# Kernel tuning notes

Measured on AMD Instinct MI355X. Metric: run time of the kernel, lower is better.

Reference implementation:

```python
import jax, jax.numpy as jnp
import numpy as np

TARGET_RADIUS = 0.99
EPS = 1e-8


def _effective_W_h(W_h):
    """Spectral-norm constraint: 3 power iterations (no grad through u,v),
    then rescale W_h so its spectral radius is TARGET_RADIUS."""
    dim = W_h.shape[0]
    u = jax.random.normal(jax.random.key(1), (dim,), dtype=W_h.dtype)
    u = u / jnp.linalg.norm(u)
    Ws = jax.lax.stop_gradient(W_h)
    v = None
    for _ in range(3):
        v = Ws.T @ u
        v = v / (jnp.linalg.norm(v) + EPS)
        u = Ws @ v
        u = u / (jnp.linalg.norm(u) + EPS)
    sigma = jnp.abs(u @ W_h @ v)  # grad flows only through W_h here
    return W_h * (TARGET_RADIUS / (sigma + EPS))


def setup_inputs() -> dict:
    key = jax.random.key(0)
    ks = jax.random.split(key, 6)
    T, B, D = 2048, 16, 1024
    xavier = float(np.sqrt(6.0 / (D + D)))
    return {
        "x": jax.random.normal(ks[0], (T, B, D), dtype=jnp.float32),
        "h0": jnp.zeros((B, D), dtype=jnp.float32),
        "W_x": jax.random.uniform(ks[1], (D, D), jnp.float32, -xavier, xavier),
        "W_h": jax.random.uniform(ks[2], (D, D), jnp.float32, -xavier, xavier),
        "W_delta": jax.random.uniform(ks[3], (D, D), jnp.float32, -0.1 * xavier, 0.1 * xavier),
        "b": jnp.zeros((D,), dtype=jnp.float32),
        "b_delta": jnp.full((D,), -2.0, dtype=jnp.float32),
        "b_gate": jnp.zeros((D,), dtype=jnp.float32),
    }


def reference(x, h0, W_x, W_h, W_delta, b, b_delta, b_gate):
    # x: [T, B, D]; h0: [B, D]
    W_h_eff = _effective_W_h(W_h)
    # Batch the input-side GEMMs over all timesteps at once.
    delta_raw = jnp.einsum("tbd,ed->tbe", x, W_delta) + b_delta  # [T,B,D]
    cand_x = jnp.einsum("tbd,ed->tbe", x, W_x) + b               # [T,B,D]

    def step(h_prev, inputs):
        x_t, dr_t, cx_t = inputs
        delta = jax.nn.sigmoid(dr_t)
        candidate = jnp.tanh(cx_t + h_prev @ W_h_eff.T)
        h_new = (1.0 - delta) * h_prev + delta * candidate
        out_t = h_new * jax.nn.silu(h_new + x_t + b_gate)
        return h_new, (out_t, h_new)

    _, (output, hs) = jax.lax.scan(step, h0, (x, delta_raw, cand_x))
    h = jnp.concatenate([h0[None], hs], axis=0)  # [T+1, B, D]
    return output, h
```

## Files before the change

kernel.cpp:

```cpp
#include <hip/hip_runtime.h>
#include <hip/hip_fp16.h>
#include <stdint.h>

#define TT 2048
#define BB 16
#define DD 1024
static const size_t H0OFF = 33554432;

typedef _Float16 f16;
typedef _Float16 f16x2 __attribute__((ext_vector_type(2)));
typedef _Float16 f16x8 __attribute__((ext_vector_type(8)));
typedef float f32x4 __attribute__((ext_vector_type(4)));

__device__ __forceinline__ float erfinv_xla(float x) {
  float w = -log1pf(-x * x);
  float p;
  if (w < 5.0f) {
    w -= 2.5f;
    p = 2.81022636e-08f;
    p = fmaf(p, w, 3.43273939e-07f);
    p = fmaf(p, w, -3.5233877e-06f);
    p = fmaf(p, w, -4.39150654e-06f);
    p = fmaf(p, w, 0.00021858087f);
    p = fmaf(p, w, -0.00125372503f);
    p = fmaf(p, w, -0.00417768164f);
    p = fmaf(p, w, 0.246640727f);
    p = fmaf(p, w, 1.50140941f);
  } else {
    w = sqrtf(w) - 3.0f;
    p = -0.000200214257f;
    p = fmaf(p, w, 0.000100950558f);
    p = fmaf(p, w, 0.00134934322f);
    p = fmaf(p, w, -0.00367342844f);
    p = fmaf(p, w, 0.00573950773f);
    p = fmaf(p, w, -0.0076224613f);
    p = fmaf(p, w, 0.00943887047f);
    p = fmaf(p, w, 1.00167406f);
    p = fmaf(p, w, 2.83297682f);
  }
  return p * x;
}

__device__ __forceinline__ float bits_to_normal(unsigned bits) {
  unsigned fb = (bits >> 9) | 0x3f800000u;
  float f = __uint_as_float(fb) - 1.0f;
  const float lo = -0.99999994f;
  float u = f * 2.0f + lo;
  u = fmaxf(lo, u);
  return __uint_as_float(0x3fb504f3u) * erfinv_xla(u);
}

#define TF_ROUND(r) { x0 += x1; x1 = (x1 << r) | (x1 >> (32 - r)); x1 ^= x0; }

__global__ void k_u0(float* t0, float* u) {
  __shared__ float red[512];
  int i = threadIdx.x;
  unsigned ks0 = 0u, ks1 = 1u, ks2 = 0x1BD11BDAu ^ 0u ^ 1u;
  unsigned x0 = (unsigned)i + ks0;
  unsigned x1 = (unsigned)(i + 512) + ks1;
  TF_ROUND(13) TF_ROUND(15) TF_ROUND(26) TF_ROUND(6)
  x0 += ks1; x1 += ks2 + 1u;
  TF_ROUND(17) TF_ROUND(29) TF_ROUND(16) TF_ROUND(24)
  x0 += ks2; x1 += ks0 + 2u;
  TF_ROUND(13) TF_ROUND(15) TF_ROUND(26) TF_ROUND(6)
  x0 += ks0; x1 += ks1 + 3u;
  TF_ROUND(17) TF_ROUND(29) TF_ROUND(16) TF_ROUND(24)
  x0 += ks1; x1 += ks2 + 4u;
  TF_ROUND(13) TF_ROUND(15) TF_ROUND(26) TF_ROUND(6)
  x0 += ks2; x1 += ks0 + 5u;
  float z0 = bits_to_normal(x0);
  float z1 = bits_to_normal(x1);
  t0[i] = z0; t0[i + 512] = z1;
  red[i] = z0 * z0 + z1 * z1;
  __syncthreads();
  for (int s = 256; s > 0; s >>= 1) { if (i < s) red[i] += red[i + s]; __syncthreads(); }
  float inv = 1.0f / sqrtf(red[0]);
  u[i] = t0[i] * inv; u[i + 512] = t0[i + 512] * inv;
}

__global__ void k_mvT(const float* __restrict__ W, const float* __restrict__ u,
                      float* __restrict__ out) {
  int j = blockIdx.x * 256 + threadIdx.x;
  float acc = 0.f;
  for (int i = 0; i < DD; ++i) acc = fmaf(W[(size_t)i * DD + j], u[i], acc);
  out[j] = acc;
}

__global__ void k_mv(const float* __restrict__ W, const float* __restrict__ v,
                     float* __restrict__ out) {
  int gtid = blockIdx.x * 256 + threadIdx.x;
  int wave = gtid >> 6, lane = threadIdx.x & 63;
  for (int rr = 0; rr < 16; ++rr) {
    int row = wave * 16 + rr;
    float acc = 0.f;
    for (int c = 0; c < 16; ++c) {
      int col = c * 64 + lane;
      acc = fmaf(W[(size_t)row * DD + col], v[col], acc);
    }
    for (int off = 32; off > 0; off >>= 1) acc += __shfl_down(acc, off, 64);
    if (lane == 0) out[row] = acc;
  }
}

__global__ void k_norm(const float* __restrict__ src, float* __restrict__ dst, float eps) {
  __shared__ float red[1024];
  int i = threadIdx.x;
  float xv = src[i];
  red[i] = xv * xv;
  __syncthreads();
  for (int s = 512; s > 0; s >>= 1) { if (i < s) red[i] += red[i + s]; __syncthreads(); }
  float inv = 1.0f / (sqrtf(red[0]) + eps);
  dst[i] = src[i] * inv;
}

__global__ void k_sigma(const float* __restrict__ u, const float* __restrict__ wv,
                        float* __restrict__ scale) {
  __shared__ float red[1024];
  int i = threadIdx.x;
  red[i] = u[i] * wv[i];
  __syncthreads();
  for (int s = 512; s > 0; s >>= 1) { if (i < s) red[i] += red[i + s]; __syncthreads(); }
  if (i == 0) scale[0] = 0.99f / (fabsf(red[0]) + 1e-8f);
}

__global__ void k_castWh(const float* __restrict__ Wh, const float* __restrict__ scale,
                         f16* __restrict__ WhH) {
  int i = blockIdx.x * 256 + threadIdx.x;
  float s = scale[0];
  WhH[i] = (f16)(Wh[i] * s);
}

__global__ __launch_bounds__(256) void k_gemm(const float* __restrict__ X,
                                              const float* __restrict__ Wt,
                                              const float* __restrict__ bias,
                                              float* __restrict__ Cout) {
  __shared__ __align__(16) f16 Ah[128 * 64];
  __shared__ __align__(16) f16 Bh[128 * 64];
  int m0 = blockIdx.x * 128, n0 = blockIdx.y * 128;
  int tid = threadIdx.x, lane = tid & 63, w = tid >> 6;
  int wm = w & 1, wn = w >> 1;
  int srow = tid >> 3, scol = (tid & 7) * 8;
  f32x4 acc[4][4];
#pragma unroll
  for (int i = 0; i < 4; ++i)
#pragma unroll
    for (int j = 0; j < 4; ++j) acc[i][j] = (f32x4){0.f, 0.f, 0.f, 0.f};

  for (int kt = 0; kt < 16; ++kt) {
    int k0 = kt * 64;
#pragma unroll
    for (int c = 0; c < 4; ++c) {
      int row = c * 32 + srow;
      const float4* sa = (const float4*)(X + (size_t)(m0 + row) * DD + k0 + scol);
      float4 a0 = sa[0], a1 = sa[1];
      f16x8 hv;
      hv[0] = (f16)a0.x; hv[1] = (f16)a0.y; hv[2] = (f16)a0.z; hv[3] = (f16)a0.w;
      hv[4] = (f16)a1.x; hv[5] = (f16)a1.y; hv[6] = (f16)a1.z; hv[7] = (f16)a1.w;
      *(f16x8*)&Ah[row * 64 + scol] = hv;
      const float4* sb = (const float4*)(Wt + (size_t)(n0 + row) * DD + k0 + scol);
      float4 b0 = sb[0], b1 = sb[1];
      f16x8 hw;
      hw[0] = (f16)b0.x; hw[1] = (f16)b0.y; hw[2] = (f16)b0.z; hw[3] = (f16)b0.w;
      hw[4] = (f16)b1.x; hw[5] = (f16)b1.y; hw[6] = (f16)b1.z; hw[7] = (f16)b1.w;
      *(f16x8*)&Bh[row * 64 + scol] = hw;
    }
    __syncthreads();
#pragma unroll
    for (int ks = 0; ks < 2; ++ks) {
      f16x8 af[4], bf[4];
#pragma unroll
      for (int i = 0; i < 4; ++i)
        af[i] = *(const f16x8*)&Ah[(wm * 64 + i * 16 + (lane & 15)) * 64 + ks * 32 + (lane >> 4) * 8];
#pragma unroll
      for (int j = 0; j < 4; ++j)
        bf[j] = *(const f16x8*)&Bh[(wn * 64 + j * 16 + (lane & 15)) * 64 + ks * 32 + (lane >> 4) * 8];
#pragma unroll
      for (int i = 0; i < 4; ++i)
#pragma unroll
        for (int j = 0; j < 4; ++j)
          acc[i][j] = __builtin_amdgcn_mfma_f32_16x16x32_f16(af[i], bf[j], acc[i][j], 0, 0, 0);
    }
    __syncthreads();
  }
#pragma unroll
  for (int j = 0; j < 4; ++j) {
    int col = n0 + wn * 64 + j * 16 + (lane & 15);
    float bs = bias[col];
#pragma unroll
    for (int i = 0; i < 4; ++i) {
      int rbase = m0 + wm * 64 + i * 16 + (lane >> 4) * 4;
#pragma unroll
      for (int r = 0; r < 4; ++r)
        Cout[(size_t)(rbase + r) * DD + col] = acc[i][j][r] + bs;
    }
  }
}

__device__ __forceinline__ float fdot2f(f16x2 a, f16x2 b, float c) {
#if __has_builtin(__builtin_amdgcn_fdot2)
  return __builtin_amdgcn_fdot2(a, b, c, false);
#else
  return c + (float)a[0] * (float)b[0] + (float)a[1] * (float)b[1];
#endif
}

__device__ __forceinline__ float sigmoid_fast(float v) {
  return 1.0f / (1.0f + __expf(-v));
}
__device__ __forceinline__ float tanh_fast(float v) {
  float t = __expf(-2.0f * fabsf(v));
  float r = (1.0f - t) / (1.0f + t);
  return copysignf(r, v);
}

__global__ __launch_bounds__(256, 1) void k_rec(const float* __restrict__ x,
                                                const float* __restrict__ h0,
                                                const float* __restrict__ b_gate,
                                                const f16* __restrict__ WhH,
                                                uint32_t* __restrict__ hx,
                                                float* __restrict__ d_out) {
  int bid = blockIdx.x;
  int batch = bid & 15;
  int eslice = bid >> 4;
  int tid = threadIdx.x, lane = tid & 63, wv = tid >> 6;
  int e0 = eslice * 64;
  int e = e0 + lane;

  __shared__ __align__(16) uint32_t hsh[512];
  __shared__ float partial[4][64];

  f16x2 wreg[128];
  const f16* wrow = WhH + (size_t)e * DD + wv * 256;
#pragma unroll
  for (int k = 0; k < 128; ++k) wreg[k] = *(const f16x2*)(wrow + 2 * k);

  {
    const float* hb = h0 + (size_t)batch * DD + 4 * tid;
    float a0 = hb[0], a1 = hb[1], a2 = hb[2], a3 = hb[3];
    f16x2 p0; p0[0] = (f16)a0; p0[1] = (f16)a1;
    f16x2 p1; p1[0] = (f16)a2; p1[1] = (f16)a3;
    hsh[2 * tid]     = __builtin_bit_cast(uint32_t, p0);
    hsh[2 * tid + 1] = __builtin_bit_cast(uint32_t, p1);
  }
  float h_own = 0.f, bgv = 0.f, cx_c = 0.f, dr_c = 0.f, xv_c = 0.f;
  if (wv == 0) {
    h_own = h0[(size_t)batch * DD + e];
    bgv = b_gate[e];
    d_out[H0OFF + (size_t)batch * DD + e] = h_own;
    size_t base0 = (size_t)batch * DD + e;
    cx_c = d_out[base0];
    dr_c = d_out[H0OFF + 16384 + base0];
    xv_c = x[base0];
  }
  __syncthreads();

#pragma unroll 1
  for (int t = 0; t < TT; ++t) {
    float cx_n = 0.f, dr_n = 0.f, xv_n = 0.f;
    if (wv == 0 && t + 1 < TT) {
      size_t basen = (size_t)(t + 1) * 16384 + (size_t)batch * DD + e;
      cx_n = d_out[basen];
      dr_n = d_out[H0OFF + 16384 + basen];
      xv_n = x[basen];
    }
    float acc = 0.f;
#pragma unroll
    for (int k4 = 0; k4 < 32; ++k4) {
      uint4 q = *(((const uint4*)hsh) + wv * 32 + k4);
      acc = fdot2f(wreg[k4 * 4 + 0], __builtin_bit_cast(f16x2, q.x), acc);
      acc = fdot2f(wreg[k4 * 4 + 1], __builtin_bit_cast(f16x2, q.y), acc);
      acc = fdot2f(wreg[k4 * 4 + 2], __builtin_bit_cast(f16x2, q.z), acc);
      acc = fdot2f(wreg[k4 * 4 + 3], __builtin_bit_cast(f16x2, q.w), acc);
    }
    partial[wv][lane] = acc;
    __syncthreads();

    uint32_t want = (uint32_t)(t + 1);
    uint32_t* slot = hx + (size_t)(want & 15u) * (BB * DD) + (size_t)batch * DD;

    if (wv == 0) {
      float hdot = partial[0][lane] + partial[1][lane] + partial[2][lane] + partial[3][lane];
      float dlt = sigmoid_fast(dr_c);
      float cand = tanh_fast(cx_c + hdot);
      float hn = (1.f - dlt) * h_own + dlt * cand;
      uint16_t hb16 = __builtin_bit_cast(uint16_t, (f16)hn);
      __hip_atomic_store(&slot[e], (want << 16) | (uint32_t)hb16,
                         __ATOMIC_RELAXED, __HIP_MEMORY_SCOPE_AGENT);
      size_t base = (size_t)t * 16384 + (size_t)batch * DD + e;
      float z = hn + xv_c + bgv;
      d_out[base] = hn * z * sigmoid_fast(z);
      d_out[H0OFF + 16384 + base] = hn;
      h_own = hn; cx_c = cx_n; dr_c = dr_n; xv_c = xv_n;
    }

    if (t + 1 < TT) {
      uint32_t* wp = slot + 4 * tid;
      uint32_t w0, w1, w2, w3;
      while (true) {
        w0 = __hip_atomic_load(wp + 0, __ATOMIC_RELAXED, __HIP_MEMORY_SCOPE_AGENT);
        w1 = __hip_atomic_load(wp + 1, __ATOMIC_RELAXED, __HIP_MEMORY_SCOPE_AGENT);
        w2 = __hip_atomic_load(wp + 2, __ATOMIC_RELAXED, __HIP_MEMORY_SCOPE_AGENT);
        w3 = __hip_atomic_load(wp + 3, __ATOMIC_RELAXED, __HIP_MEMORY_SCOPE_AGENT);
        if (((w0 >> 16) == want) && ((w1 >> 16) == want) &&
            ((w2 >> 16) == want) && ((w3 >> 16) == want)) break;
      }
      hsh[2 * tid]     = (w0 & 0xffffu) | (w1 << 16);
      hsh[2 * tid + 1] = (w2 & 0xffffu) | (w3 << 16);
      __syncthreads();
    }
  }
}

extern "C" void kernel_launch(void* const* d_in, const int* in_sizes, int n_in,
                              void* d_out_v, int out_size, void* d_ws, size_t ws_size,
                              hipStream_t stream) {
  const float* x  = (const float*)d_in[0];
  const float* h0 = (const float*)d_in[1];
  const float* Wx = (const float*)d_in[2];
  const float* Wh = (const float*)d_in[3];
  const float* Wd = (const float*)d_in[4];
  const float* b  = (const float*)d_in[5];
  const float* bd = (const float*)d_in[6];
  const float* bg = (const float*)d_in[7];
  float* out = (float*)d_out_v;

  char* ws = (char*)d_ws;
  float* u    = (float*)(ws + 0);
  float* v    = (float*)(ws + 4096);
  float* t0   = (float*)(ws + 8192);
  float* sc   = (float*)(ws + 12288);
  uint32_t* hx = (uint32_t*)(ws + 65536);
  f16* WhH  = (f16*)(ws + 2097152);

  hipMemsetAsync(hx, 0, (size_t)16 * BB * DD * 4, stream);

  k_u0<<<1, 512, 0, stream>>>(t0, u);
  for (int it = 0; it < 3; ++it) {
    k_mvT<<<4, 256, 0, stream>>>(Wh, u, t0);
    k_norm<<<1, 1024, 0, stream>>>(t0, v, 1e-8f);
    k_mv<<<16, 256, 0, stream>>>(Wh, v, t0);
    k_norm<<<1, 1024, 0, stream>>>(t0, u, 1e-8f);
  }
  k_sigma<<<1, 1024, 0, stream>>>(u, t0, sc);
  k_castWh<<<4096, 256, 0, stream>>>(Wh, sc, WhH);

  dim3 gg(256, 8, 1);
  k_gemm<<<gg, 256, 0, stream>>>(x, Wx, b, out);
  k_gemm<<<gg, 256, 0, stream>>>(x, Wd, bd, out + H0OFF + 16384);

  k_rec<<<256, 256, 0, stream>>>(x, h0, bg, WhH, hx, out);
}
```

Measured before the change: 4.262 ms.

## Make recurrent h exchange wave-local and spread the step epilogue across all waves

Each wave now polls and loads only the 256-element slice of the new hidden state that its own dot products use, and writes it to its own region of shared memory. This drops the block-wide barrier at the end of every timestep, and the partial-sum buffer is double-buffered so a single barrier per step is enough. The per-element epilogue work is split across 16 lanes of each of the four waves instead of running only in wave 0. The dot product uses four independent accumulators for more instruction-level parallelism. Polling becomes a two-phase wave-uniform check with s_sleep, which may add some wake-up latency on the critical path.

```diff
diff --git a/kernel.cpp b/kernel.cpp
--- a/kernel.cpp
+++ b/kernel.cpp
@@ -196,11 +196,13 @@
   }
 }
 
-__device__ __forceinline__ float fdot2f(f16x2 a, f16x2 b, float c) {
+__device__ __forceinline__ float fdot2u(uint32_t a, uint32_t b, float c) {
 #if __has_builtin(__builtin_amdgcn_fdot2)
-  return __builtin_amdgcn_fdot2(a, b, c, false);
+  return __builtin_amdgcn_fdot2(__builtin_bit_cast(f16x2, a),
+                                __builtin_bit_cast(f16x2, b), c, false);
 #else
-  return c + (float)a[0] * (float)b[0] + (float)a[1] * (float)b[1];
+  f16x2 av = __builtin_bit_cast(f16x2, a), bv = __builtin_bit_cast(f16x2, b);
+  return c + (float)av[0] * (float)bv[0] + (float)av[1] * (float)bv[1];
 #endif
 }
 
@@ -223,70 +225,90 @@
   int batch = bid & 15;
   int eslice = bid >> 4;
   int tid = threadIdx.x, lane = tid & 63, wv = tid >> 6;
-  int e0 = eslice * 64;
-  int e = e0 + lane;
-
-  __shared__ __align__(16) uint32_t hsh[512];
-  __shared__ float partial[4][64];
-
-  f16x2 wreg[128];
-  const f16* wrow = WhH + (size_t)e * DD + wv * 256;
-#pragma unroll
-  for (int k = 0; k < 128; ++k) wreg[k] = *(const f16x2*)(wrow + 2 * k);
-
+
+  __shared__ __align__(16) uint16_t hsh[1024];
+  __shared__ float partial[2][4][64];
+
+  uint4 wq[32];
   {
-    const float* hb = h0 + (size_t)batch * DD + 4 * tid;
-    float a0 = hb[0], a1 = hb[1], a2 = hb[2], a3 = hb[3];
-    f16x2 p0; p0[0] = (f16)a0; p0[1] = (f16)a1;
-    f16x2 p1; p1[0] = (f16)a2; p1[1] = (f16)a3;
-    hsh[2 * tid]     = __builtin_bit_cast(uint32_t, p0);
-    hsh[2 * tid + 1] = __builtin_bit_cast(uint32_t, p1);
-  }
+    const uint4* wp = (const uint4*)(WhH + (size_t)(64 * eslice + lane) * DD + 256 * wv);
+#pragma unroll
+    for (int k = 0; k < 32; ++k) wq[k] = wp[k];
+  }
+
+#pragma unroll
+  for (int k = 0; k < 4; ++k) {
+    int g = 256 * wv + 64 * k + lane;
+    hsh[g] = __builtin_bit_cast(uint16_t, (f16)h0[(size_t)batch * DD + g]);
+  }
+
   float h_own = 0.f, bgv = 0.f, cx_c = 0.f, dr_c = 0.f, xv_c = 0.f;
-  if (wv == 0) {
-    h_own = h0[(size_t)batch * DD + e];
-    bgv = b_gate[e];
-    d_out[H0OFF + (size_t)batch * DD + e] = h_own;
-    size_t base0 = (size_t)batch * DD + e;
-    cx_c = d_out[base0];
-    dr_c = d_out[H0OFF + 16384 + base0];
-    xv_c = x[base0];
-  }
-  __syncthreads();
+  int e_g = 0;
+  if (lane < 16) {
+    int rr = 16 * wv + lane;
+    e_g = 64 * eslice + rr;
+    size_t b0 = (size_t)batch * DD + e_g;
+    h_own = h0[b0];
+    bgv = b_gate[e_g];
+    d_out[H0OFF + b0] = h_own;
+    cx_c = d_out[b0];
+    dr_c = d_out[H0OFF + 16384 + b0];
+    xv_c = x[b0];
+  }
+  asm volatile("s_waitcnt lgkmcnt(0)" ::: "memory");
 
 #pragma unroll 1
   for (int t = 0; t < TT; ++t) {
     float cx_n = 0.f, dr_n = 0.f, xv_n = 0.f;
-    if (wv == 0 && t + 1 < TT) {
-      size_t basen = (size_t)(t + 1) * 16384 + (size_t)batch * DD + e;
-      cx_n = d_out[basen];
-      dr_n = d_out[H0OFF + 16384 + basen];
-      xv_n = x[basen];
-    }
-    float acc = 0.f;
-#pragma unroll
-    for (int k4 = 0; k4 < 32; ++k4) {
-      uint4 q = *(((const uint4*)hsh) + wv * 32 + k4);
-      acc = fdot2f(wreg[k4 * 4 + 0], __builtin_bit_cast(f16x2, q.x), acc);
-      acc = fdot2f(wreg[k4 * 4 + 1], __builtin_bit_cast(f16x2, q.y), acc);
-      acc = fdot2f(wreg[k4 * 4 + 2], __builtin_bit_cast(f16x2, q.z), acc);
-      acc = fdot2f(wreg[k4 * 4 + 3], __builtin_bit_cast(f16x2, q.w), acc);
-    }
-    partial[wv][lane] = acc;
+    if (lane < 16 && t + 1 < TT) {
+      size_t bn = (size_t)(t + 1) * 16384 + (size_t)batch * DD + e_g;
+      cx_n = d_out[bn];
+      dr_n = d_out[H0OFF + 16384 + bn];
+      xv_n = x[bn];
+    }
+
+    const uint4* hq = (const uint4*)hsh;
+    float a0 = 0.f, a1 = 0.f, a2 = 0.f, a3 = 0.f;
+#pragma unroll
+    for (int k = 0; k < 32; k += 4) {
+      {
+        uint4 q = hq[32 * wv + k + 0]; uint4 wqq = wq[k + 0];
+        a0 = fdot2u(wqq.x, q.x, a0); a0 = fdot2u(wqq.y, q.y, a0);
+        a0 = fdot2u(wqq.z, q.z, a0); a0 = fdot2u(wqq.w, q.w, a0);
+      }
+      {
+        uint4 q = hq[32 * wv + k + 1]; uint4 wqq = wq[k + 1];
+        a1 = fdot2u(wqq.x, q.x, a1); a1 = fdot2u(wqq.y, q.y, a1);
+        a1 = fdot2u(wqq.z, q.z, a1); a1 = fdot2u(wqq.w, q.w, a1);
+      }
+      {
+        uint4 q = hq[32 * wv + k + 2]; uint4 wqq = wq[k + 2];
+        a2 = fdot2u(wqq.x, q.x, a2); a2 = fdot2u(wqq.y, q.y, a2);
+        a2 = fdot2u(wqq.z, q.z, a2); a2 = fdot2u(wqq.w, q.w, a2);
+      }
+      {
+        uint4 q = hq[32 * wv + k + 3]; uint4 wqq = wq[k + 3];
+        a3 = fdot2u(wqq.x, q.x, a3); a3 = fdot2u(wqq.y, q.y, a3);
+        a3 = fdot2u(wqq.z, q.z, a3); a3 = fdot2u(wqq.w, q.w, a3);
+      }
+    }
+    partial[t & 1][wv][lane] = (a0 + a1) + (a2 + a3);
     __syncthreads();
 
     uint32_t want = (uint32_t)(t + 1);
-    uint32_t* slot = hx + (size_t)(want & 15u) * (BB * DD) + (size_t)batch * DD;
-
-    if (wv == 0) {
-      float hdot = partial[0][lane] + partial[1][lane] + partial[2][lane] + partial[3][lane];
+    uint32_t* sl = hx + (size_t)(want & 15u) * (BB * DD) + (size_t)batch * DD;
+
+    if (lane < 16) {
+      int rr = 16 * wv + lane;
+      const float* pp = &partial[t & 1][0][rr];
+      float hdot = (pp[0] + pp[64]) + (pp[128] + pp[192]);
       float dlt = sigmoid_fast(dr_c);
       float cand = tanh_fast(cx_c + hdot);
       float hn = (1.f - dlt) * h_own + dlt * cand;
-      uint16_t hb16 = __builtin_bit_cast(uint16_t, (f16)hn);
-      __hip_atomic_store(&slot[e], (want << 16) | (uint32_t)hb16,
+      uint16_t hb = __builtin_bit_cast(uint16_t, (f16)hn);
+      __hip_atomic_store(&sl[e_g], (want << 16) | (uint32_t)hb,
                          __ATOMIC_RELAXED, __HIP_MEMORY_SCOPE_AGENT);
-      size_t base = (size_t)t * 16384 + (size_t)batch * DD + e;
+      size_t base = (size_t)t * 16384 + (size_t)batch * DD + e_g;
       float z = hn + xv_c + bgv;
       d_out[base] = hn * z * sigmoid_fast(z);
       d_out[H0OFF + 16384 + base] = hn;
@@ -294,19 +316,30 @@
     }
 
     if (t + 1 < TT) {
-      uint32_t* wp = slot + 4 * tid;
-      uint32_t w0, w1, w2, w3;
+      int sidx = 256 * wv + 64 * (lane >> 2) + 16 * (lane & 3);
       while (true) {
-        w0 = __hip_atomic_load(wp + 0, __ATOMIC_RELAXED, __HIP_MEMORY_SCOPE_AGENT);
-        w1 = __hip_atomic_load(wp + 1, __ATOMIC_RELAXED, __HIP_MEMORY_SCOPE_AGENT);
-        w2 = __hip_atomic_load(wp + 2, __ATOMIC_RELAXED, __HIP_MEMORY_SCOPE_AGENT);
-        w3 = __hip_atomic_load(wp + 3, __ATOMIC_RELAXED, __HIP_MEMORY_SCOPE_AGENT);
-        if (((w0 >> 16) == want) && ((w1 >> 16) == want) &&
-            ((w2 >> 16) == want) && ((w3 >> 16) == want)) break;
-      }
-      hsh[2 * tid]     = (w0 & 0xffffu) | (w1 << 16);
-      hsh[2 * tid + 1] = (w2 & 0xffffu) | (w3 << 16);
-      __syncthreads();
+        uint32_t swd = (lane < 16)
+            ? __hip_atomic_load(&sl[sidx], __ATOMIC_RELAXED, __HIP_MEMORY_SCOPE_AGENT)
+            : (want << 16);
+        if (__all((swd >> 16) == want)) break;
+        __builtin_amdgcn_s_sleep(1);
+      }
+      uint32_t v0, v1, v2, v3;
+      while (true) {
+        v0 = __hip_atomic_load(&sl[256 * wv + lane],       __ATOMIC_RELAXED, __HIP_MEMORY_SCOPE_AGENT);
+        v1 = __hip_atomic_load(&sl[256 * wv + 64 + lane],  __ATOMIC_RELAXED, __HIP_MEMORY_SCOPE_AGENT);
+        v2 = __hip_atomic_load(&sl[256 * wv + 128 + lane], __ATOMIC_RELAXED, __HIP_MEMORY_SCOPE_AGENT);
+        v3 = __hip_atomic_load(&sl[256 * wv + 192 + lane], __ATOMIC_RELAXED, __HIP_MEMORY_SCOPE_AGENT);
+        bool ok = ((v0 >> 16) == want) & ((v1 >> 16) == want) &
+                  ((v2 >> 16) == want) & ((v3 >> 16) == want);
+        if (__all(ok)) break;
+        __builtin_amdgcn_s_sleep(1);
+      }
+      hsh[256 * wv + lane]       = (uint16_t)v0;
+      hsh[256 * wv + 64 + lane]  = (uint16_t)v1;
+      hsh[256 * wv + 128 + lane] = (uint16_t)v2;
+      hsh[256 * wv + 192 + lane] = (uint16_t)v3;
+      asm volatile("s_waitcnt lgkmcnt(0)" ::: "memory");
     }
   }
 }
```

After: 4.890 ms. 14.7% more time.

## Move recurrent weights from registers to transposed LDS and split accumulators

Applied to the files above, without the earlier changes.

Stores each block's 64-row slice of the fp16 recurrent weight matrix transposed in shared memory instead of holding 128 packed values per thread in registers. The dot product reads weights from LDS and uses four independent accumulators to break the fdot2 dependency chain. The spin-wait becomes wave-uniform via __all, and the state update uses an fma. This relieves register pressure but adds an LDS load per fdot2 on the serial per-timestep critical path and needs 128KB of LDS.

```diff
diff --git a/kernel.cpp b/kernel.cpp
--- a/kernel.cpp
+++ b/kernel.cpp
@@ -196,11 +196,13 @@
   }
 }
 
-__device__ __forceinline__ float fdot2f(f16x2 a, f16x2 b, float c) {
+__device__ __forceinline__ float fdot2u(uint32_t a, uint32_t b, float c) {
 #if __has_builtin(__builtin_amdgcn_fdot2)
-  return __builtin_amdgcn_fdot2(a, b, c, false);
+  return __builtin_amdgcn_fdot2(__builtin_bit_cast(f16x2, a),
+                                __builtin_bit_cast(f16x2, b), c, false);
 #else
-  return c + (float)a[0] * (float)b[0] + (float)a[1] * (float)b[1];
+  f16x2 av = __builtin_bit_cast(f16x2, a), bv = __builtin_bit_cast(f16x2, b);
+  return c + (float)av[0] * (float)bv[0] + (float)av[1] * (float)bv[1];
 #endif
 }
 
@@ -223,70 +225,80 @@
   int batch = bid & 15;
   int eslice = bid >> 4;
   int tid = threadIdx.x, lane = tid & 63, wv = tid >> 6;
-  int e0 = eslice * 64;
-  int e = e0 + lane;
-
-  __shared__ __align__(16) uint32_t hsh[512];
+
+  __shared__ uint32_t WT[512 * 64];
+  __shared__ __align__(16) uint16_t hsh[1024];
   __shared__ float partial[4][64];
 
-  f16x2 wreg[128];
-  const f16* wrow = WhH + (size_t)e * DD + wv * 256;
-#pragma unroll
-  for (int k = 0; k < 128; ++k) wreg[k] = *(const f16x2*)(wrow + 2 * k);
-
+  {
+    int r = tid >> 2, q = tid & 3;
+    const uint32_t* src = (const uint32_t*)(WhH + (size_t)(64 * eslice + r) * DD) + q * 128;
+#pragma unroll 8
+    for (int j = 0; j < 128; ++j)
+      WT[(q * 128 + j) * 64 + r] = src[j];
+  }
   {
     const float* hb = h0 + (size_t)batch * DD + 4 * tid;
     float a0 = hb[0], a1 = hb[1], a2 = hb[2], a3 = hb[3];
-    f16x2 p0; p0[0] = (f16)a0; p0[1] = (f16)a1;
-    f16x2 p1; p1[0] = (f16)a2; p1[1] = (f16)a3;
-    hsh[2 * tid]     = __builtin_bit_cast(uint32_t, p0);
-    hsh[2 * tid + 1] = __builtin_bit_cast(uint32_t, p1);
-  }
+    uint32_t lo = ((uint32_t)__builtin_bit_cast(uint16_t, (f16)a0)) |
+                  ((uint32_t)__builtin_bit_cast(uint16_t, (f16)a1) << 16);
+    uint32_t hi = ((uint32_t)__builtin_bit_cast(uint16_t, (f16)a2)) |
+                  ((uint32_t)__builtin_bit_cast(uint16_t, (f16)a3) << 16);
+    uint2 pk; pk.x = lo; pk.y = hi;
+    ((uint2*)hsh)[tid] = pk;
+  }
+
   float h_own = 0.f, bgv = 0.f, cx_c = 0.f, dr_c = 0.f, xv_c = 0.f;
+  int e_g = 64 * eslice + lane;
   if (wv == 0) {
-    h_own = h0[(size_t)batch * DD + e];
-    bgv = b_gate[e];
-    d_out[H0OFF + (size_t)batch * DD + e] = h_own;
-    size_t base0 = (size_t)batch * DD + e;
-    cx_c = d_out[base0];
-    dr_c = d_out[H0OFF + 16384 + base0];
-    xv_c = x[base0];
+    size_t b0 = (size_t)batch * DD + e_g;
+    h_own = h0[b0];
+    bgv = b_gate[e_g];
+    d_out[H0OFF + b0] = h_own;
+    cx_c = d_out[b0];
+    dr_c = d_out[H0OFF + 16384 + b0];
+    xv_c = x[b0];
   }
   __syncthreads();
+
+  const uint4* hq4 = (const uint4*)hsh;
 
 #pragma unroll 1
   for (int t = 0; t < TT; ++t) {
     float cx_n = 0.f, dr_n = 0.f, xv_n = 0.f;
     if (wv == 0 && t + 1 < TT) {
-      size_t basen = (size_t)(t + 1) * 16384 + (size_t)batch * DD + e;
-      cx_n = d_out[basen];
-      dr_n = d_out[H0OFF + 16384 + basen];
-      xv_n = x[basen];
-    }
-    float acc = 0.f;
-#pragma unroll
-    for (int k4 = 0; k4 < 32; ++k4) {
-      uint4 q = *(((const uint4*)hsh) + wv * 32 + k4);
-      acc = fdot2f(wreg[k4 * 4 + 0], __builtin_bit_cast(f16x2, q.x), acc);
-      acc = fdot2f(wreg[k4 * 4 + 1], __builtin_bit_cast(f16x2, q.y), acc);
-      acc = fdot2f(wreg[k4 * 4 + 2], __builtin_bit_cast(f16x2, q.z), acc);
-      acc = fdot2f(wreg[k4 * 4 + 3], __builtin_bit_cast(f16x2, q.w), acc);
-    }
-    partial[wv][lane] = acc;
+      size_t bn = (size_t)(t + 1) * 16384 + (size_t)batch * DD + e_g;
+      cx_n = d_out[bn];
+      dr_n = d_out[H0OFF + 16384 + bn];
+      xv_n = x[bn];
+    }
+
+    float a0 = 0.f, a1 = 0.f, a2 = 0.f, a3 = 0.f;
+#pragma unroll
+    for (int k = 0; k < 32; ++k) {
+      uint4 hh = hq4[32 * wv + k];
+      int d4 = 128 * wv + 4 * k;
+      a0 = fdot2u(WT[(d4 + 0) * 64 + lane], hh.x, a0);
+      a1 = fdot2u(WT[(d4 + 1) * 64 + lane], hh.y, a1);
+      a2 = fdot2u(WT[(d4 + 2) * 64 + lane], hh.z, a2);
+      a3 = fdot2u(WT[(d4 + 3) * 64 + lane], hh.w, a3);
+    }
+    partial[wv][lane] = (a0 + a1) + (a2 + a3);
     __syncthreads();
 
     uint32_t want = (uint32_t)(t + 1);
     uint32_t* slot = hx + (size_t)(want & 15u) * (BB * DD) + (size_t)batch * DD;
 
     if (wv == 0) {
-      float hdot = partial[0][lane] + partial[1][lane] + partial[2][lane] + partial[3][lane];
+      float hdot = (partial[0][lane] + partial[1][lane]) +
+                   (partial[2][lane] + partial[3][lane]);
       float dlt = sigmoid_fast(dr_c);
       float cand = tanh_fast(cx_c + hdot);
-      float hn = (1.f - dlt) * h_own + dlt * cand;
-      uint16_t hb16 = __builtin_bit_cast(uint16_t, (f16)hn);
-      __hip_atomic_store(&slot[e], (want << 16) | (uint32_t)hb16,
+      float hn = fmaf(dlt, cand - h_own, h_own);
+      uint16_t hb = __builtin_bit_cast(uint16_t, (f16)hn);
+      __hip_atomic_store(&slot[e_g], (want << 16) | (uint32_t)hb,
                          __ATOMIC_RELAXED, __HIP_MEMORY_SCOPE_AGENT);
-      size_t base = (size_t)t * 16384 + (size_t)batch * DD + e;
+      size_t base = (size_t)t * 16384 + (size_t)batch * DD + e_g;
       float z = hn + xv_c + bgv;
       d_out[base] = hn * z * sigmoid_fast(z);
       d_out[H0OFF + 16384 + base] = hn;
@@ -301,11 +313,14 @@
         w1 = __hip_atomic_load(wp + 1, __ATOMIC_RELAXED, __HIP_MEMORY_SCOPE_AGENT);
         w2 = __hip_atomic_load(wp + 2, __ATOMIC_RELAXED, __HIP_MEMORY_SCOPE_AGENT);
         w3 = __hip_atomic_load(wp + 3, __ATOMIC_RELAXED, __HIP_MEMORY_SCOPE_AGENT);
-        if (((w0 >> 16) == want) && ((w1 >> 16) == want) &&
-            ((w2 >> 16) == want) && ((w3 >> 16) == want)) break;
+        bool ok = ((w0 >> 16) == want) & ((w1 >> 16) == want) &
+                  ((w2 >> 16) == want) & ((w3 >> 16) == want);
+        if (__all(ok)) break;
       }
-      hsh[2 * tid]     = (w0 & 0xffffu) | (w1 << 16);
-      hsh[2 * tid + 1] = (w2 & 0xffffu) | (w3 << 16);
+      uint2 pk;
+      pk.x = (w0 & 0xffffu) | (w1 << 16);
+      pk.y = (w2 & 0xffffu) | (w3 << 16);
+      ((uint2*)hsh)[tid] = pk;
       __syncthreads();
     }
   }
```

Measured after the change: 5.038 ms. 18.2% more time.
